# Optimization experiments

Measured on AMD Instinct MI355X. Metric: run time of the kernel, lower is better.

The kernel has to match this reference:

```python
import jax, jax.numpy as jnp
import numpy as np

M, N, DIM, B = 64, 64, 512, 4096
SIGMA = max(M, N) / 2.0  # default sigma in BaseSOM.__init__


def setup_inputs() -> dict:
    key = jax.random.key(0)
    k1, k2 = jax.random.split(key)
    batch = jax.random.normal(k1, (B, DIM), dtype=jnp.float32)
    weights = jax.random.uniform(k2, (M * N, DIM), dtype=jnp.float32)
    # grid locations [(i, j) for i in range(M) for j in range(N)]
    ii, jj = jnp.meshgrid(jnp.arange(M), jnp.arange(N), indexing="ij")
    locations = jnp.stack([ii.reshape(-1), jj.reshape(-1)], axis=1).astype(jnp.int64)
    return {
        "batch": batch,
        "weights": weights,
        "locations": locations,
        "decay_rate": 1000,
        "it": 100,
    }


def reference(batch, weights, locations, decay_rate, it):
    # Squared Euclidean distances (argmin is identical to argmin of cdist p=2).
    x2 = jnp.sum(batch * batch, axis=1, keepdims=True)          # [B, 1]
    w2 = jnp.sum(weights * weights, axis=1)[None, :]            # [1, MN]
    d2 = x2 - 2.0 * (batch @ weights.T) + w2                    # [B, MN]
    bmu_indices = jnp.argmin(d2, axis=1)                        # [B]
    bmu_loc = locations[bmu_indices]                            # [B, 2]
    lr = jnp.exp(-jnp.float32(it) / jnp.float32(decay_rate))
    sigma_op = jnp.float32(SIGMA) * lr
    # [B, MN, 2] grid offsets -> squared grid distance [B, MN]
    diff = locations[None, :, :].astype(jnp.float32) - bmu_loc[:, None, :].astype(jnp.float32)
    dist_sq = jnp.sum(diff * diff, axis=2)
    return jnp.exp(-dist_sq / (sigma_op * sigma_op))
```

## Files before the change

### kernel.cpp

```cpp
#include <hip/hip_runtime.h>
#include <cfloat>

#define DIMK 512
#define MN   4096
#define BATCH 4096
#define NGRP 1024

typedef _Float16 half8_t __attribute__((ext_vector_type(8)));
typedef _Float16 half4_t __attribute__((ext_vector_type(4)));
typedef float f32x4 __attribute__((ext_vector_type(4)));

#define GLD16(gp, lp) __builtin_amdgcn_global_load_lds( \
    (const __attribute__((address_space(1))) void*)(gp), \
    (__attribute__((address_space(3))) void*)(lp), 16, 0, 0)

__global__ __launch_bounds__(256) void convert_kernel(
        const float* __restrict__ X, const float* __restrict__ W,
        _Float16* __restrict__ Xh, _Float16* __restrict__ Wh,
        float* __restrict__ w2, float* __restrict__ xnorm) {
    const int blk  = blockIdx.x;
    const int t    = threadIdx.x;
    const bool isW = blk >= 1024;
    const float* src = isW ? W : X;
    _Float16* dst  = isW ? Wh : Xh;
    const int rblk = isW ? blk - 1024 : blk;
    const size_t idx = (size_t)rblk * 2048 + (size_t)t * 8;

    float4 v0 = *(const float4*)(src + idx);
    float4 v1 = *(const float4*)(src + idx + 4);
    float v[8] = {v0.x, v0.y, v0.z, v0.w, v1.x, v1.y, v1.z, v1.w};
    half8_t hv;
    float s = 0.f;
#pragma unroll
    for (int e = 0; e < 8; e++) {
        s += v[e] * v[e];
        hv[e] = (_Float16)v[e];
    }
    *(half8_t*)(dst + idx) = hv;
#pragma unroll
    for (int o = 32; o > 0; o >>= 1) s += __shfl_down(s, o);
    if ((t & 63) == 0) {
        int row = rblk * 4 + (t >> 6);
        if (isW) w2[row] = s;
        else     xnorm[row] = __fsqrt_rn(s);
    }
}

#define MFMA16(A0, A1, A2, A3, R) \
    do { \
        acc[(R)+0][0] = __builtin_amdgcn_mfma_f32_16x16x32_f16(A0, b0, acc[(R)+0][0], 0, 0, 0); \
        acc[(R)+0][1] = __builtin_amdgcn_mfma_f32_16x16x32_f16(A0, b1, acc[(R)+0][1], 0, 0, 0); \
        acc[(R)+0][2] = __builtin_amdgcn_mfma_f32_16x16x32_f16(A0, b2, acc[(R)+0][2], 0, 0, 0); \
        acc[(R)+0][3] = __builtin_amdgcn_mfma_f32_16x16x32_f16(A0, b3, acc[(R)+0][3], 0, 0, 0); \
        acc[(R)+1][0] = __builtin_amdgcn_mfma_f32_16x16x32_f16(A1, b0, acc[(R)+1][0], 0, 0, 0); \
        acc[(R)+1][1] = __builtin_amdgcn_mfma_f32_16x16x32_f16(A1, b1, acc[(R)+1][1], 0, 0, 0); \
        acc[(R)+1][2] = __builtin_amdgcn_mfma_f32_16x16x32_f16(A1, b2, acc[(R)+1][2], 0, 0, 0); \
        acc[(R)+1][3] = __builtin_amdgcn_mfma_f32_16x16x32_f16(A1, b3, acc[(R)+1][3], 0, 0, 0); \
        acc[(R)+2][0] = __builtin_amdgcn_mfma_f32_16x16x32_f16(A2, b0, acc[(R)+2][0], 0, 0, 0); \
        acc[(R)+2][1] = __builtin_amdgcn_mfma_f32_16x16x32_f16(A2, b1, acc[(R)+2][1], 0, 0, 0); \
        acc[(R)+2][2] = __builtin_amdgcn_mfma_f32_16x16x32_f16(A2, b2, acc[(R)+2][2], 0, 0, 0); \
        acc[(R)+2][3] = __builtin_amdgcn_mfma_f32_16x16x32_f16(A2, b3, acc[(R)+2][3], 0, 0, 0); \
        acc[(R)+3][0] = __builtin_amdgcn_mfma_f32_16x16x32_f16(A3, b0, acc[(R)+3][0], 0, 0, 0); \
        acc[(R)+3][1] = __builtin_amdgcn_mfma_f32_16x16x32_f16(A3, b1, acc[(R)+3][1], 0, 0, 0); \
        acc[(R)+3][2] = __builtin_amdgcn_mfma_f32_16x16x32_f16(A3, b2, acc[(R)+3][2], 0, 0, 0); \
        acc[(R)+3][3] = __builtin_amdgcn_mfma_f32_16x16x32_f16(A3, b3, acc[(R)+3][3], 0, 0, 0); \
    } while (0)

__global__ __launch_bounds__(512, 2) void score_kernel(
        const _Float16* __restrict__ Xh, const _Float16* __restrict__ Wh,
        const float* __restrict__ w2, _Float16* __restrict__ Gm) {
    __shared__ __align__(16) _Float16 lds[4][2][8192];

    const int t    = threadIdx.x;
    const int lane = t & 63;
    const int w    = t >> 6;
    const int wm   = w >> 2;
    const int wn   = w & 3;

    const int id  = blockIdx.y * 16 + blockIdx.x;
    const int xcd = id & 7;
    const int li  = id >> 3;
    const int bm  = (xcd >> 1) * 4 + (li >> 3);
    const int bn  = (xcd & 1) * 8 + (li & 7);
    const int m0  = bm * 256;
    const int n0  = bn * 256;

    const int srow = (t >> 6) * 16 + (t & 15);
    const int skof = ((t >> 4) & 3) * 8;
    const _Float16* gA = Xh + (size_t)(m0 + srow) * DIMK + skof;
    const _Float16* gB = Wh + (size_t)(n0 + srow) * DIMK + skof;
    const int ldst = t * 8;

#define STG_A(bf, kt, c) GLD16(gA + (size_t)(c) * (128 * DIMK) + (kt) * 32, &lds[bf][0][(c) * 4096 + ldst])
#define STG_B(bf, kt, c) GLD16(gB + (size_t)(c) * (128 * DIMK) + (kt) * 32, &lds[bf][1][(c) * 4096 + ldst])
#define LDA(bf, rg) (*(const half8_t*)(&lds[bf][0][(rg) * 512 + lane * 8]))
#define LDB(bf, rg) (*(const half8_t*)(&lds[bf][1][(rg) * 512 + lane * 8]))

    f32x4 acc[8][4];
#pragma unroll
    for (int i = 0; i < 8; i++)
#pragma unroll
        for (int j = 0; j < 4; j++) acc[i][j] = (f32x4){0.f, 0.f, 0.f, 0.f};

    STG_A(0, 0, 0); STG_A(0, 0, 1); STG_B(0, 0, 0); STG_B(0, 0, 1);
    STG_A(1, 1, 0); STG_A(1, 1, 1); STG_B(1, 1, 0); STG_B(1, 1, 1);
    STG_A(2, 2, 0); STG_A(2, 2, 1); STG_B(2, 2, 0); STG_B(2, 2, 1);

#pragma unroll
    for (int kt = 0; kt < 16; ++kt) {
        const int bf = kt & 3;
        const int nb = (kt + 3) & 3;

        if (kt <= 13)      { asm volatile("s_waitcnt vmcnt(8)" ::: "memory"); }
        else if (kt == 14) { asm volatile("s_waitcnt vmcnt(4)" ::: "memory"); }
        else               { asm volatile("s_waitcnt vmcnt(0)" ::: "memory"); }
        __builtin_amdgcn_sched_barrier(0);
        __builtin_amdgcn_s_barrier();

        if (kt <= 12) { STG_A(nb, kt + 3, 0); STG_A(nb, kt + 3, 1); }

        half8_t a0 = LDA(bf, wm * 8 + 0), a1 = LDA(bf, wm * 8 + 1);
        half8_t a2 = LDA(bf, wm * 8 + 2), a3 = LDA(bf, wm * 8 + 3);
        half8_t b0 = LDB(bf, wn * 4 + 0), b1 = LDB(bf, wn * 4 + 1);
        half8_t b2 = LDB(bf, wn * 4 + 2), b3 = LDB(bf, wn * 4 + 3);
        half8_t a4 = LDA(bf, wm * 8 + 4), a5 = LDA(bf, wm * 8 + 5);
        half8_t a6 = LDA(bf, wm * 8 + 6), a7 = LDA(bf, wm * 8 + 7);

        if (kt <= 12) { STG_B(nb, kt + 3, 0); STG_B(nb, kt + 3, 1); }

        asm volatile("s_waitcnt lgkmcnt(4)" ::: "memory");
        __builtin_amdgcn_sched_barrier(0);
        __builtin_amdgcn_s_setprio(1);
        MFMA16(a0, a1, a2, a3, 0);
        __builtin_amdgcn_s_setprio(0);

        asm volatile("s_waitcnt lgkmcnt(0)" ::: "memory");
        __builtin_amdgcn_sched_barrier(0);
        __builtin_amdgcn_s_setprio(1);
        MFMA16(a4, a5, a6, a7, 4);
        __builtin_amdgcn_s_setprio(0);
    }

    const int q   = lane >> 4;
    const int cl  = lane & 15;
    const int gb  = (n0 >> 2) + wn * 16;
    float w2v[4];
#pragma unroll
    for (int j = 0; j < 4; j++) w2v[j] = w2[n0 + wn * 64 + j * 16 + cl];
#pragma unroll
    for (int ai = 0; ai < 8; ai++)
#pragma unroll
        for (int v = 0; v < 4; v++) {
            const int row = m0 + wm * 128 + ai * 16 + q * 4 + v;
            _Float16* grow = Gm + (size_t)row * 1024 + gb;
#pragma unroll
            for (int j = 0; j < 4; j++) {
                float s = w2v[j] - 2.0f * acc[ai][j][v];
                s = fminf(s, __shfl_xor(s, 1));
                s = fminf(s, __shfl_xor(s, 2));
                if ((cl & 3) == 0) grow[j * 4 + (cl >> 2)] = (_Float16)s;
            }
        }
}

__global__ __launch_bounds__(256) void argmin_kernel(
        const float* __restrict__ w2, const float* __restrict__ xnorm,
        const float* __restrict__ X, const float* __restrict__ W,
        const _Float16* __restrict__ gm, int* __restrict__ bmu) {
    __shared__ float xs[512];
    __shared__ int   list[NGRP];
    __shared__ int   cnt;
    __shared__ float wmin[4];
    __shared__ unsigned long long wkey[4];
    const int row  = blockIdx.x;
    const int t    = threadIdx.x;
    const int lane = t & 63;
    const int w    = t >> 6;

    {
        float2 xv = *(const float2*)(X + (size_t)row * DIMK + t * 2);
        xs[2 * t]     = xv.x;
        xs[2 * t + 1] = xv.y;
    }
    if (t == 0) cnt = 0;

    half4_t gmh = *((const half4_t*)(gm + (size_t)row * 1024) + t);
    float gme[4] = {(float)gmh[0], (float)gmh[1], (float)gmh[2], (float)gmh[3]};
    float g = fminf(fminf(gme[0], gme[1]), fminf(gme[2], gme[3]));
#pragma unroll
    for (int mask = 1; mask <= 32; mask <<= 1)
        g = fminf(g, __shfl_xor(g, mask));
    if (lane == 0) wmin[w] = g;
    __syncthreads();
    const float gmin = fminf(fminf(wmin[0], wmin[1]), fminf(wmin[2], wmin[3]));
    const float tau  = gmin + 2.0f * (0.0222f * xnorm[row] + 0.25f);

#pragma unroll
    for (int e = 0; e < 4; e++)
        if (gme[e] <= tau) list[atomicAdd(&cnt, 1)] = t * 4 + e;
    __syncthreads();
    const int total = cnt;

    const int s16 = lane & 15;
    const int cg  = lane >> 4;
    float4 xq[8];
#pragma unroll
    for (int e = 0; e < 8; e++) xq[e] = ((const float4*)xs)[e * 16 + s16];

    unsigned long long mkey = ~0ULL;
    for (int idx = w; idx < total; idx += 4) {
        const int col = list[idx] * 4 + cg;
        const float4* wr = (const float4*)(W + (size_t)col * DIMK);
        float p = 0.f;
#pragma unroll
        for (int e = 0; e < 8; e++) {
            float4 wv = wr[e * 16 + s16];
            p += xq[e].x * wv.x + xq[e].y * wv.y
               + xq[e].z * wv.z + xq[e].w * wv.w;
        }
        p += __shfl_xor(p, 1); p += __shfl_xor(p, 2);
        p += __shfl_xor(p, 4); p += __shfl_xor(p, 8);
        const float s = w2[col] - 2.0f * p;
        unsigned int b = __float_as_uint(s);
        unsigned int u = (b & 0x80000000u) ? ~b : (b | 0x80000000u);
        unsigned long long key = ((unsigned long long)u << 32) | (unsigned int)col;
        mkey = key < mkey ? key : mkey;
    }
    {
        unsigned long long o;
        o = __shfl_xor(mkey, 16); mkey = o < mkey ? o : mkey;
        o = __shfl_xor(mkey, 32); mkey = o < mkey ? o : mkey;
    }
    if (lane == 0) wkey[w] = mkey;
    __syncthreads();
    if (t == 0) {
        unsigned long long k = wkey[0];
#pragma unroll
        for (int i = 1; i < 4; i++) k = wkey[i] < k ? wkey[i] : k;
        bmu[row] = (int)(k & 0xffffffffu);
    }
}

__global__ __launch_bounds__(256) void gauss_kernel(
        const int* __restrict__ bmu, const int* __restrict__ decay_p,
        const int* __restrict__ it_p, float* __restrict__ out) {
    __shared__ float tab[128];
    const int row = blockIdx.x;
    const int t   = threadIdx.x;
    const int sbi = bmu[row];

    const float lr  = __expf(-(float)(*it_p) / (float)(*decay_p));
    const float so  = 32.0f * lr;
    const float inv = 1.0f / (so * so);
    const int rr = sbi >> 6, cc = sbi & 63;
    if (t < 64) {
        float d = (float)(t - rr);
        tab[t] = __expf(-d * d * inv);
    } else if (t < 128) {
        float d = (float)(t - 64 - cc);
        tab[t] = __expf(-d * d * inv);
    }
    __syncthreads();
    const float* er = tab;
    const float* ec = tab + 64;
    f32x4* orow = (f32x4*)(out + (size_t)row * 4096);
#pragma unroll
    for (int qq = 0; qq < 4; qq++) {
        int f  = qq * 256 + t;
        int i  = f >> 4;
        int j0 = (f & 15) * 4;
        float e = er[i];
        f32x4 o = {e * ec[j0], e * ec[j0 + 1], e * ec[j0 + 2], e * ec[j0 + 3]};
        __builtin_nontemporal_store(o, orow + f);
    }
}

extern "C" void kernel_launch(void* const* d_in, const int* in_sizes, int n_in,
                              void* d_out, int out_size, void* d_ws, size_t ws_size,
                              hipStream_t stream) {
    const float* X       = (const float*)d_in[0];
    const float* W       = (const float*)d_in[1];
    const int*   decay_p = (const int*)d_in[3];
    const int*   it_p    = (const int*)d_in[4];
    float* out = (float*)d_out;

    _Float16* Xh = (_Float16*)d_ws;
    _Float16* Wh = Xh + (size_t)BATCH * DIMK;
    float*    w2 = (float*)(Wh + (size_t)MN * DIMK);
    float*    xn = w2 + MN;
    _Float16* gmv = (_Float16*)(xn + BATCH);
    int*      bmu = (int*)(gmv + (size_t)BATCH * 1024);

    convert_kernel<<<2048, 256, 0, stream>>>(X, W, Xh, Wh, w2, xn);
    score_kernel<<<dim3(16, 16), 512, 0, stream>>>(Xh, Wh, w2, gmv);
    argmin_kernel<<<BATCH, 256, 0, stream>>>(w2, xn, X, W, gmv, bmu);
    gauss_kernel<<<BATCH, 256, 0, stream>>>(bmu, decay_p, it_p, out);
}
```

Baseline: 137.0 us.

## Shrink score GEMM tiles to 128x128 and fuse argmin with gaussian output kernel

The score GEMM moves from 256x256 tiles with 512 threads and 4-stage LDS buffering to 128x128 tiles with 256 threads, 3 stages and 3 blocks per CU. This gives 1024 blocks instead of 256, which should fill the 256 CUs and balance load better. The cost is less data reuse per tile and a shallower prefetch pipeline. Separately, the argmin and gaussian kernels are fused into one epilogue kernel, which removes one launch and the bmu round trip through global memory.

```diff
diff --git a/kernel.cpp b/kernel.cpp
--- a/kernel.cpp
+++ b/kernel.cpp
@@ -46,44 +46,24 @@
     }
 }
 
-#define MFMA16(A0, A1, A2, A3, R) \
-    do { \
-        acc[(R)+0][0] = __builtin_amdgcn_mfma_f32_16x16x32_f16(A0, b0, acc[(R)+0][0], 0, 0, 0); \
-        acc[(R)+0][1] = __builtin_amdgcn_mfma_f32_16x16x32_f16(A0, b1, acc[(R)+0][1], 0, 0, 0); \
-        acc[(R)+0][2] = __builtin_amdgcn_mfma_f32_16x16x32_f16(A0, b2, acc[(R)+0][2], 0, 0, 0); \
-        acc[(R)+0][3] = __builtin_amdgcn_mfma_f32_16x16x32_f16(A0, b3, acc[(R)+0][3], 0, 0, 0); \
-        acc[(R)+1][0] = __builtin_amdgcn_mfma_f32_16x16x32_f16(A1, b0, acc[(R)+1][0], 0, 0, 0); \
-        acc[(R)+1][1] = __builtin_amdgcn_mfma_f32_16x16x32_f16(A1, b1, acc[(R)+1][1], 0, 0, 0); \
-        acc[(R)+1][2] = __builtin_amdgcn_mfma_f32_16x16x32_f16(A1, b2, acc[(R)+1][2], 0, 0, 0); \
-        acc[(R)+1][3] = __builtin_amdgcn_mfma_f32_16x16x32_f16(A1, b3, acc[(R)+1][3], 0, 0, 0); \
-        acc[(R)+2][0] = __builtin_amdgcn_mfma_f32_16x16x32_f16(A2, b0, acc[(R)+2][0], 0, 0, 0); \
-        acc[(R)+2][1] = __builtin_amdgcn_mfma_f32_16x16x32_f16(A2, b1, acc[(R)+2][1], 0, 0, 0); \
-        acc[(R)+2][2] = __builtin_amdgcn_mfma_f32_16x16x32_f16(A2, b2, acc[(R)+2][2], 0, 0, 0); \
-        acc[(R)+2][3] = __builtin_amdgcn_mfma_f32_16x16x32_f16(A2, b3, acc[(R)+2][3], 0, 0, 0); \
-        acc[(R)+3][0] = __builtin_amdgcn_mfma_f32_16x16x32_f16(A3, b0, acc[(R)+3][0], 0, 0, 0); \
-        acc[(R)+3][1] = __builtin_amdgcn_mfma_f32_16x16x32_f16(A3, b1, acc[(R)+3][1], 0, 0, 0); \
-        acc[(R)+3][2] = __builtin_amdgcn_mfma_f32_16x16x32_f16(A3, b2, acc[(R)+3][2], 0, 0, 0); \
-        acc[(R)+3][3] = __builtin_amdgcn_mfma_f32_16x16x32_f16(A3, b3, acc[(R)+3][3], 0, 0, 0); \
-    } while (0)
-
-__global__ __launch_bounds__(512, 2) void score_kernel(
+__global__ __launch_bounds__(256, 3) void score_kernel(
         const _Float16* __restrict__ Xh, const _Float16* __restrict__ Wh,
         const float* __restrict__ w2, _Float16* __restrict__ Gm) {
-    __shared__ __align__(16) _Float16 lds[4][2][8192];
+    __shared__ __align__(16) _Float16 lds[3][2][4096];
 
     const int t    = threadIdx.x;
     const int lane = t & 63;
     const int w    = t >> 6;
-    const int wm   = w >> 2;
-    const int wn   = w & 3;
-
-    const int id  = blockIdx.y * 16 + blockIdx.x;
+    const int wm   = w >> 1;
+    const int wn   = w & 1;
+
+    const int id  = blockIdx.y * 32 + blockIdx.x;
     const int xcd = id & 7;
     const int li  = id >> 3;
-    const int bm  = (xcd >> 1) * 4 + (li >> 3);
-    const int bn  = (xcd & 1) * 8 + (li & 7);
-    const int m0  = bm * 256;
-    const int n0  = bn * 256;
+    const int bm  = xcd * 4 + (li >> 5);
+    const int bn  = li & 31;
+    const int m0  = bm * 128;
+    const int n0  = bn * 128;
 
     const int srow = (t >> 6) * 16 + (t & 15);
     const int skof = ((t >> 4) & 3) * 8;
@@ -91,53 +71,51 @@
     const _Float16* gB = Wh + (size_t)(n0 + srow) * DIMK + skof;
     const int ldst = t * 8;
 
-#define STG_A(bf, kt, c) GLD16(gA + (size_t)(c) * (128 * DIMK) + (kt) * 32, &lds[bf][0][(c) * 4096 + ldst])
-#define STG_B(bf, kt, c) GLD16(gB + (size_t)(c) * (128 * DIMK) + (kt) * 32, &lds[bf][1][(c) * 4096 + ldst])
+#define STG_A(bf, kt, c) GLD16(gA + (size_t)(c) * (64 * DIMK) + (kt) * 32, &lds[bf][0][(c) * 2048 + ldst])
+#define STG_B(bf, kt, c) GLD16(gB + (size_t)(c) * (64 * DIMK) + (kt) * 32, &lds[bf][1][(c) * 2048 + ldst])
 #define LDA(bf, rg) (*(const half8_t*)(&lds[bf][0][(rg) * 512 + lane * 8]))
 #define LDB(bf, rg) (*(const half8_t*)(&lds[bf][1][(rg) * 512 + lane * 8]))
 
-    f32x4 acc[8][4];
-#pragma unroll
-    for (int i = 0; i < 8; i++)
+    f32x4 acc[4][4];
+#pragma unroll
+    for (int i = 0; i < 4; i++)
 #pragma unroll
         for (int j = 0; j < 4; j++) acc[i][j] = (f32x4){0.f, 0.f, 0.f, 0.f};
 
     STG_A(0, 0, 0); STG_A(0, 0, 1); STG_B(0, 0, 0); STG_B(0, 0, 1);
     STG_A(1, 1, 0); STG_A(1, 1, 1); STG_B(1, 1, 0); STG_B(1, 1, 1);
-    STG_A(2, 2, 0); STG_A(2, 2, 1); STG_B(2, 2, 0); STG_B(2, 2, 1);
 
 #pragma unroll
     for (int kt = 0; kt < 16; ++kt) {
-        const int bf = kt & 3;
-        const int nb = (kt + 3) & 3;
-
-        if (kt <= 13)      { asm volatile("s_waitcnt vmcnt(8)" ::: "memory"); }
-        else if (kt == 14) { asm volatile("s_waitcnt vmcnt(4)" ::: "memory"); }
-        else               { asm volatile("s_waitcnt vmcnt(0)" ::: "memory"); }
+        const int bf = kt % 3;
+        const int nb = (kt + 2) % 3;
+
+        if (kt <= 14) { asm volatile("s_waitcnt vmcnt(4)" ::: "memory"); }
+        else          { asm volatile("s_waitcnt vmcnt(0)" ::: "memory"); }
         __builtin_amdgcn_sched_barrier(0);
         __builtin_amdgcn_s_barrier();
 
-        if (kt <= 12) { STG_A(nb, kt + 3, 0); STG_A(nb, kt + 3, 1); }
-
-        half8_t a0 = LDA(bf, wm * 8 + 0), a1 = LDA(bf, wm * 8 + 1);
-        half8_t a2 = LDA(bf, wm * 8 + 2), a3 = LDA(bf, wm * 8 + 3);
+        if (kt <= 13) {
+            STG_A(nb, kt + 2, 0); STG_A(nb, kt + 2, 1);
+            STG_B(nb, kt + 2, 0); STG_B(nb, kt + 2, 1);
+        }
+
+        half8_t a0 = LDA(bf, wm * 4 + 0), a1 = LDA(bf, wm * 4 + 1);
+        half8_t a2 = LDA(bf, wm * 4 + 2), a3 = LDA(bf, wm * 4 + 3);
         half8_t b0 = LDB(bf, wn * 4 + 0), b1 = LDB(bf, wn * 4 + 1);
         half8_t b2 = LDB(bf, wn * 4 + 2), b3 = LDB(bf, wn * 4 + 3);
-        half8_t a4 = LDA(bf, wm * 8 + 4), a5 = LDA(bf, wm * 8 + 5);
-        half8_t a6 = LDA(bf, wm * 8 + 6), a7 = LDA(bf, wm * 8 + 7);
-
-        if (kt <= 12) { STG_B(nb, kt + 3, 0); STG_B(nb, kt + 3, 1); }
-
-        asm volatile("s_waitcnt lgkmcnt(4)" ::: "memory");
-        __builtin_amdgcn_sched_barrier(0);
-        __builtin_amdgcn_s_setprio(1);
-        MFMA16(a0, a1, a2, a3, 0);
-        __builtin_amdgcn_s_setprio(0);
 
         asm volatile("s_waitcnt lgkmcnt(0)" ::: "memory");
         __builtin_amdgcn_sched_barrier(0);
         __builtin_amdgcn_s_setprio(1);
-        MFMA16(a4, a5, a6, a7, 4);
+#pragma unroll
+        for (int i = 0; i < 4; i++) {
+            half8_t av = (i == 0) ? a0 : (i == 1) ? a1 : (i == 2) ? a2 : a3;
+            acc[i][0] = __builtin_amdgcn_mfma_f32_16x16x32_f16(av, b0, acc[i][0], 0, 0, 0);
+            acc[i][1] = __builtin_amdgcn_mfma_f32_16x16x32_f16(av, b1, acc[i][1], 0, 0, 0);
+            acc[i][2] = __builtin_amdgcn_mfma_f32_16x16x32_f16(av, b2, acc[i][2], 0, 0, 0);
+            acc[i][3] = __builtin_amdgcn_mfma_f32_16x16x32_f16(av, b3, acc[i][3], 0, 0, 0);
+        }
         __builtin_amdgcn_s_setprio(0);
     }
 
@@ -148,14 +126,14 @@
 #pragma unroll
     for (int j = 0; j < 4; j++) w2v[j] = w2[n0 + wn * 64 + j * 16 + cl];
 #pragma unroll
-    for (int ai = 0; ai < 8; ai++)
+    for (int i = 0; i < 4; i++)
 #pragma unroll
         for (int v = 0; v < 4; v++) {
-            const int row = m0 + wm * 128 + ai * 16 + q * 4 + v;
+            const int row = m0 + wm * 64 + i * 16 + q * 4 + v;
             _Float16* grow = Gm + (size_t)row * 1024 + gb;
 #pragma unroll
             for (int j = 0; j < 4; j++) {
-                float s = w2v[j] - 2.0f * acc[ai][j][v];
+                float s = w2v[j] - 2.0f * acc[i][j][v];
                 s = fminf(s, __shfl_xor(s, 1));
                 s = fminf(s, __shfl_xor(s, 2));
                 if ((cl & 3) == 0) grow[j * 4 + (cl >> 2)] = (_Float16)s;
@@ -163,15 +141,18 @@
         }
 }
 
-__global__ __launch_bounds__(256) void argmin_kernel(
+__global__ __launch_bounds__(256) void epilogue_kernel(
         const float* __restrict__ w2, const float* __restrict__ xnorm,
         const float* __restrict__ X, const float* __restrict__ W,
-        const _Float16* __restrict__ gm, int* __restrict__ bmu) {
+        const _Float16* __restrict__ gm,
+        const int* __restrict__ decay_p, const int* __restrict__ it_p,
+        float* __restrict__ out) {
     __shared__ float xs[512];
     __shared__ int   list[NGRP];
     __shared__ int   cnt;
     __shared__ float wmin[4];
     __shared__ unsigned long long wkey[4];
+    __shared__ float tab[128];
     const int row  = blockIdx.x;
     const int t    = threadIdx.x;
     const int lane = t & 63;
@@ -233,21 +214,10 @@
     }
     if (lane == 0) wkey[w] = mkey;
     __syncthreads();
-    if (t == 0) {
-        unsigned long long k = wkey[0];
-#pragma unroll
-        for (int i = 1; i < 4; i++) k = wkey[i] < k ? wkey[i] : k;
-        bmu[row] = (int)(k & 0xffffffffu);
-    }
-}
-
-__global__ __launch_bounds__(256) void gauss_kernel(
-        const int* __restrict__ bmu, const int* __restrict__ decay_p,
-        const int* __restrict__ it_p, float* __restrict__ out) {
-    __shared__ float tab[128];
-    const int row = blockIdx.x;
-    const int t   = threadIdx.x;
-    const int sbi = bmu[row];
+    unsigned long long k = wkey[0];
+#pragma unroll
+    for (int i = 1; i < 4; i++) k = wkey[i] < k ? wkey[i] : k;
+    const int sbi = (int)(k & 0xffffffffu);
 
     const float lr  = __expf(-(float)(*it_p) / (float)(*decay_p));
     const float so  = 32.0f * lr;
@@ -289,10 +259,8 @@
     float*    w2 = (float*)(Wh + (size_t)MN * DIMK);
     float*    xn = w2 + MN;
     _Float16* gmv = (_Float16*)(xn + BATCH);
-    int*      bmu = (int*)(gmv + (size_t)BATCH * 1024);
 
     convert_kernel<<<2048, 256, 0, stream>>>(X, W, Xh, Wh, w2, xn);
-    score_kernel<<<dim3(16, 16), 512, 0, stream>>>(Xh, Wh, w2, gmv);
-    argmin_kernel<<<BATCH, 256, 0, stream>>>(w2, xn, X, W, gmv, bmu);
-    gauss_kernel<<<BATCH, 256, 0, stream>>>(bmu, decay_p, it_p, out);
-}
+    score_kernel<<<dim3(32, 32), 256, 0, stream>>>(Xh, Wh, w2, gmv);
+    epilogue_kernel<<<BATCH, 256, 0, stream>>>(w2, xn, X, W, gmv, decay_p, it_p, out);
+}
```

After: 141.9 us. 3.6% more time.
